# Performance work log

Measured on AMD Instinct MI355X. Metric: run time of the kernel, lower is better.

The kernel has to match this reference:

```python
import jax, jax.numpy as jnp
import numpy as np
from jax import lax

KS = 5            # patch kernel size
STRIDE = 4        # patch stride / scale ratio
SHIFTS = (2, 2)   # roll shifts before patch extraction
SOFTMAX_SCALE = 10.0
MID_CH = 64
BAND_HS = 8


def same_pad(x, k, s):
    """TensorFlow-style SAME padding for kernel k, stride s (NCHW)."""
    H, W = x.shape[-2], x.shape[-1]
    oh, ow = -(-H // s), -(-W // s)
    ph = max(0, (oh - 1) * s + k - H)
    pw = max(0, (ow - 1) * s + k - W)
    return jnp.pad(x, ((0, 0), (0, 0), (ph // 2, ph - ph // 2), (pw // 2, pw - pw // 2)))


def extract_patches(x, k, s, shifts):
    """torch.nn.Unfold equivalent with SAME padding and roll -> [N, L, C, k, k]."""
    x = same_pad(x, k, s)
    x = jnp.roll(x, shifts[0], axis=2)
    x = jnp.roll(x, shifts[1], axis=3)
    p = lax.conv_general_dilated_patches(
        x, (k, k), (s, s), 'VALID', dimension_numbers=('NCHW', 'OIHW', 'NCHW'))
    N, _, Hn, Wn = p.shape
    C = x.shape[1]
    # channel ordering is (C, kh, kw) channel-slowest, matching torch unfold
    return p.reshape(N, C, k, k, Hn * Wn).transpose(0, 4, 1, 2, 3)


def conv3(x, w, b):
    """3x3 conv, padding=1, bias + LeakyReLU(0.01) (BasicBlock)."""
    y = lax.conv_general_dilated(x, w, (1, 1), [(1, 1), (1, 1)],
                                 dimension_numbers=('NCHW', 'OIHW', 'NCHW'))
    return jax.nn.leaky_relu(y + b[None, :, None, None], 0.01)


def setup_inputs() -> dict:
    key = jax.random.key(0)
    ks = jax.random.split(key, 11)
    f32 = jnp.float32
    return {
        'ms':   jax.random.normal(ks[0], (2, BAND_HS, 96, 96), f32),
        'pan':  jax.random.normal(ks[1], (2, 1, 384, 384), f32),
        'pan2': jax.random.normal(ks[2], (2, 1, 96, 96), f32),
        'wq': jax.random.normal(ks[3], (MID_CH, 1, 3, 3), f32) * 0.1,
        'bq': jax.random.normal(ks[4], (MID_CH,), f32) * 0.02,
        'wk': jax.random.normal(ks[5], (MID_CH, 1, 3, 3), f32) * 0.1,
        'bk': jax.random.normal(ks[6], (MID_CH,), f32) * 0.02,
        'wv': jax.random.normal(ks[7], (BAND_HS, BAND_HS, 3, 3), f32) * 0.1,
        'bv': jax.random.normal(ks[8], (BAND_HS,), f32) * 0.02,
        'wr': jax.random.normal(ks[9], (BAND_HS, BAND_HS, 3, 3), f32) * 0.1,
        'br': jax.random.normal(ks[10], (BAND_HS,), f32) * 0.02,
    }


def reference(ms, pan, pan2, wq, bq, wk, bk, wv, bv, wr, br):
    k_fea = conv3(pan2, wk, bk)                       # [N, mid, h, w]
    q_fea = conv3(pan, wq, bq)                        # [N, mid, H, W]
    v_fea = conv3(ms, wv, bv)                         # [N, band, h, w]

    k_patch = extract_patches(k_fea, KS, STRIDE, SHIFTS)  # [N, L, mid, ks, ks]
    v_patch = extract_patches(v_fea, KS, STRIDE, SHIFTS)  # [N, L, band, ks, ks]

    def attend(q, kp, vp):
        # q: [mid, H, W]; kp: [L, mid, ks, ks]; vp: [L, band, ks, ks]
        norms = jnp.sqrt(jnp.sum(kp * kp, axis=(1, 2, 3)))      # per-patch L2 norms
        k0 = kp / jnp.max(norms)                                # global-max normalization
        q0 = same_pad(q[None], KS, STRIDE)                      # [1, mid, Hp, Wp]
        scores = lax.conv_general_dilated(
            q0, k0, (STRIDE, STRIDE), 'VALID',
            dimension_numbers=('NCHW', 'OIHW', 'NCHW'))          # [1, L, H', W']
        attn = jax.nn.softmax(scores * SOFTMAX_SCALE, axis=1)
        # conv_transpose2d(attn, vp, stride) == dilated conv with flipped, transposed kernel
        wT = jnp.flip(vp, (2, 3)).transpose(1, 0, 2, 3)          # [band, L, ks, ks]
        out = lax.conv_general_dilated(
            attn, wT, (1, 1), [(KS - 1, KS - 1)] * 2,
            lhs_dilation=(STRIDE, STRIDE),
            dimension_numbers=('NCHW', 'OIHW', 'NCHW'))          # [1, band, Ho, Wo]
        return out[0] / 6.0

    res = jax.vmap(attend)(q_fea, k_patch, v_patch)   # [N, band, Ho, Wo]
    return conv3(res, wr, br)
```

## Files before the change

### kernel.cpp

```cpp
#include <hip/hip_runtime.h>
#include <math.h>


typedef _Float16 f16;
typedef _Float16 f16x8 __attribute__((ext_vector_type(8)));
typedef float f32x4 __attribute__((ext_vector_type(4)));

namespace csa {
constexpr int NB   = 2;
constexpr int MID  = 64;
constexpr int BAND = 8;
constexpr int HK   = 96;
constexpr int HQ   = 384;
constexpr int HQP  = 385;
constexpr int XI   = 97;
constexpr int LN   = 24;
constexpr int L    = 576;
constexpr int LP   = 640;
constexpr int PS   = 96 * 96;
constexpr int KDIM = MID * 25;
constexpr int VDIM = BAND * 25;
constexpr int MV   = 256;
constexpr int HO   = 385;
constexpr size_t QPSN = (size_t)4 * HQP * XI * MID;

constexpr size_t align256(size_t x) { return (x + 255) & ~(size_t)255; }
constexpr size_t OFF_QPS  = 0;
constexpr size_t OFF_KCL  = align256(OFF_QPS + (size_t)NB*QPSN*2);
constexpr size_t OFF_VFEA = align256(OFF_KCL + (size_t)NB*HK*HK*MID*2);
constexpr size_t OFF_N2   = align256(OFF_VFEA + (size_t)NB*BAND*HK*HK*4);
constexpr size_t OFF_SC   = align256(OFF_N2   + (size_t)NB*L*4);
constexpr size_t OFF_KM   = align256(OFF_SC   + 256);
constexpr size_t OFF_VT   = align256(OFF_KM   + (size_t)NB*LP*KDIM*2);
constexpr size_t OFF_ST   = align256(OFF_VT   + (size_t)NB*MV*L*2);
constexpr size_t OFF_AT   = align256(OFF_ST   + (size_t)NB*PS*LP*4);
constexpr size_t OFF_D    = align256(OFF_AT   + (size_t)NB*PS*L*2);
constexpr size_t OFF_RES  = align256(OFF_D    + (size_t)NB*MV*PS*4);
}
using namespace csa;

__global__ __launch_bounds__(256) void csa_convq_ps(
    const float* __restrict__ in, const float* __restrict__ w,
    const float* __restrict__ b, f16* __restrict__ out) {
  int id = blockIdx.x * 256 + threadIdx.x;
  int total = NB * 4 * HQP * XI;
  if (id >= total) return;
  int xi = id % XI;
  int t = id / XI;
  int yp = t % HQP;
  t /= HQP;
  int f = t % 4;
  int n = t / 4;
  int xp = 4 * xi + f;
  f16* op = out + (size_t)id * MID;
  if (yp >= HQ || xp >= HQ) {
    f16x8 z = {0, 0, 0, 0, 0, 0, 0, 0};
#pragma unroll
    for (int c8 = 0; c8 < 8; ++c8) *(f16x8*)(op + c8 * 8) = z;
    return;
  }
  const float* ip = in + (size_t)n * HQ * HQ;
  float p[9];
#pragma unroll
  for (int dy = 0; dy < 3; ++dy)
#pragma unroll
    for (int dx = 0; dx < 3; ++dx) {
      int yy = yp + dy - 1, xx = xp + dx - 1;
      p[dy * 3 + dx] = (yy >= 0 && yy < HQ && xx >= 0 && xx < HQ)
                           ? ip[(size_t)yy * HQ + xx] : 0.f;
    }
#pragma unroll
  for (int c8 = 0; c8 < 8; ++c8) {
    f16x8 o;
#pragma unroll
    for (int e = 0; e < 8; ++e) {
      int co = c8 * 8 + e;
      float acc = b[co];
#pragma unroll
      for (int k = 0; k < 9; ++k) acc = fmaf(p[k], w[co * 9 + k], acc);
      o[e] = (f16)(acc > 0.f ? acc : 0.01f * acc);
    }
    *(f16x8*)(op + c8 * 8) = o;
  }
}

__global__ __launch_bounds__(256) void csa_conv_cl(
    const float* __restrict__ in, const float* __restrict__ w,
    const float* __restrict__ b, f16* __restrict__ out, int H) {
  int id = blockIdx.x * 256 + threadIdx.x;
  int total = NB * H * H;
  if (id >= total) return;
  int x = id % H;
  int t = id / H;
  int y = t % H;
  int n = t / H;
  f16* op = out + (size_t)id * MID;
  const float* ip = in + (size_t)n * H * H;
  float p[9];
#pragma unroll
  for (int dy = 0; dy < 3; ++dy)
#pragma unroll
    for (int dx = 0; dx < 3; ++dx) {
      int yy = y + dy - 1, xx = x + dx - 1;
      p[dy * 3 + dx] = (yy >= 0 && yy < H && xx >= 0 && xx < H)
                           ? ip[(size_t)yy * H + xx] : 0.f;
    }
#pragma unroll
  for (int c8 = 0; c8 < 8; ++c8) {
    f16x8 o;
#pragma unroll
    for (int e = 0; e < 8; ++e) {
      int co = c8 * 8 + e;
      float acc = b[co];
#pragma unroll
      for (int k = 0; k < 9; ++k) acc = fmaf(p[k], w[co * 9 + k], acc);
      o[e] = (f16)(acc > 0.f ? acc : 0.01f * acc);
    }
    *(f16x8*)(op + c8 * 8) = o;
  }
}

__global__ __launch_bounds__(256) void csa_conv3_8x8(
    const float* __restrict__ in, const float* __restrict__ w,
    const float* __restrict__ b, float* __restrict__ out, int H, int W) {
  int id = blockIdx.x * 256 + threadIdx.x;
  int total = NB * H * W;
  if (id >= total) return;
  int x = id % W;
  int t = id / W;
  int y = t % H;
  int n = t / H;
  const float* ip = in + (size_t)n * BAND * H * W;
  float p[BAND][9];
#pragma unroll
  for (int ci = 0; ci < BAND; ++ci)
#pragma unroll
    for (int dy = 0; dy < 3; ++dy)
#pragma unroll
      for (int dx = 0; dx < 3; ++dx) {
        int yy = y + dy - 1, xx = x + dx - 1;
        p[ci][dy * 3 + dx] = (yy >= 0 && yy < H && xx >= 0 && xx < W)
                                 ? ip[((size_t)ci * H + yy) * W + xx] : 0.f;
      }
  float* op = out + ((size_t)n * BAND * H + y) * W + x;
  for (int co = 0; co < BAND; ++co) {
    float acc = b[co];
#pragma unroll
    for (int ci = 0; ci < BAND; ++ci)
#pragma unroll
      for (int k = 0; k < 9; ++k)
        acc = fmaf(p[ci][k], w[(co * BAND + ci) * 9 + k], acc);
    acc = acc > 0.f ? acc : 0.01f * acc;
    op[(size_t)co * H * W] = acc;
  }
}

__global__ __launch_bounds__(256) void csa_build_patches(
    const f16* __restrict__ kcl, const float* __restrict__ v_fea,
    f16* __restrict__ Kmat, f16* __restrict__ Vt, float* __restrict__ n2) {
  int blk = blockIdx.x;
  int n = blk / LP;
  int l = blk % LP;
  int tid = threadIdx.x;
  f16* krow = Kmat + ((size_t)n * LP + l) * KDIM;
  if (l >= L) {
    f16x8 z = {0, 0, 0, 0, 0, 0, 0, 0};
    for (int ch = tid; ch < 200; ch += 256) *(f16x8*)(krow + ch * 8) = z;
    return;
  }
  int i = l / LN, j = l % LN;
  const f16* kn = kcl + (size_t)n * HK * HK * MID;
  float ss = 0.f;
  for (int ch = tid; ch < 200; ch += 256) {
    int khkw = ch >> 3;
    int c0 = (ch & 7) * 8;
    int kh = khkw / 5, kw = khkw % 5;
    int r = (4 * i + kh + 95) % 97;
    int cc = (4 * j + kw + 95) % 97;
    f16x8 v = {0, 0, 0, 0, 0, 0, 0, 0};
    if (r < HK && cc < HK)
      v = *(const f16x8*)(kn + ((size_t)r * HK + cc) * MID + c0);
#pragma unroll
    for (int e = 0; e < 8; ++e) {
      float fv = (float)v[e];
      ss += fv * fv;
    }
    *(f16x8*)(krow + ch * 8) = v;
  }
  for (int m = tid; m < MV; m += 256) {
    float v = 0.f;
    if (m < VDIM) {
      int kw = m % 5;
      int t = m / 5;
      int kh = t % 5;
      int c = t / 5;
      int r = (4 * i + kh + 95) % 97;
      int cc = (4 * j + kw + 95) % 97;
      v = (r < HK && cc < HK)
              ? v_fea[(((size_t)n * BAND + c) * HK + r) * HK + cc] : 0.f;
    }
    Vt[((size_t)n * MV + m) * L + l] = (f16)v;
  }
  __shared__ float red[256];
  red[tid] = ss;
  __syncthreads();
  for (int s = 128; s > 0; s >>= 1) {
    if (tid < s) red[tid] += red[tid + s];
    __syncthreads();
  }
  if (tid == 0) n2[n * L + l] = red[0];
}

__global__ __launch_bounds__(256) void csa_max_scale(
    const float* __restrict__ n2, float* __restrict__ scale) {
  int n = blockIdx.x;
  int tid = threadIdx.x;
  float m = 0.f;
  for (int l = tid; l < L; l += 256) m = fmaxf(m, n2[n * L + l]);
  __shared__ float red[256];
  red[tid] = m;
  __syncthreads();
  for (int s = 128; s > 0; s >>= 1) {
    if (tid < s) red[tid] = fmaxf(red[tid], red[tid + s]);
    __syncthreads();
  }
  if (tid == 0) scale[n] = 10.f / sqrtf(red[0]);
}

__device__ __forceinline__ void gl_lds16(const f16* g, f16* s) {
  __builtin_amdgcn_global_load_lds(
      (const __attribute__((address_space(1))) void*)g,
      (__attribute__((address_space(3))) void*)s, 16, 0, 0);
}

__global__ __launch_bounds__(256) void csa_gemm1(
    const f16* __restrict__ qps, const f16* __restrict__ Km,
    float* __restrict__ C) {
  __shared__ __attribute__((aligned(16))) f16 As[4096];
  __shared__ __attribute__((aligned(16))) f16 Bs[4096];
  const int tid = threadIdx.x;
  const int w = tid >> 6;
  const int l = tid & 63;
  const int q = l >> 4;
  const int r = l & 15;
  const int nb = blockIdx.z;
  qps += (size_t)nb * QPSN;
  Km += (size_t)nb * LP * KDIM;
  C += (size_t)nb * (size_t)PS * LP;
  const int bm = blockIdx.y * 128;
  const int bn = blockIdx.x * 128;
  const int wm = (w >> 1) * 64;
  const int wn = (w & 1) * 64;

  f32x4 acc[4][4];
#pragma unroll
  for (int i = 0; i < 4; ++i)
#pragma unroll
    for (int j = 0; j < 4; ++j) {
      f32x4 z = {0.f, 0.f, 0.f, 0.f};
      acc[i][j] = z;
    }

  const int pg0 = bm + w * 16;
  const int y0 = pg0 / 96, x0 = pg0 % 96;
  const int pg1 = pg0 + 64;
  const int y1 = pg1 / 96, x1 = pg1 % 96;
  const int la = r * MID + q * 8;

  const f16* gb0 = Km + (size_t)(bn + w * 16 + r) * KDIM + q * 8;
  const f16* gb1 = gb0 + (size_t)64 * KDIM;
  f16* lA0 = As + w * 512;
  f16* lA1 = As + 2048 + w * 512;
  f16* lB0 = Bs + w * 512;
  f16* lB1 = Bs + 2048 + w * 512;
  const int am = (w >> 1) * 4;
  const int bnn = (w & 1) * 4;

  int t = 0;
  for (int kh = 0; kh < 5; ++kh) {
    for (int kw = 0; kw < 5; ++kw) {
      const size_t u0 =
          (((size_t)(kw & 3) * HQP + (4 * y0 + kh)) * XI + x0 + (kw >> 2)) * MID;
      const size_t u1 =
          (((size_t)(kw & 3) * HQP + (4 * y1 + kh)) * XI + x1 + (kw >> 2)) * MID;
#pragma unroll
      for (int half = 0; half < 2; ++half, ++t) {
        const size_t oA = (size_t)half * 32 + la;
        const size_t oB = (size_t)t * 32;
        gl_lds16(qps + u0 + oA, lA0);
        gl_lds16(qps + u1 + oA, lA1);
        gl_lds16(gb0 + oB, lB0);
        gl_lds16(gb1 + oB, lB1);
        __syncthreads();
        f16x8 af[4], bf[4];
#pragma unroll
        for (int u = 0; u < 4; ++u) {
          af[u] = *(const f16x8*)&As[(am + u) * 512 + q * 128 + r * 8];
          bf[u] = *(const f16x8*)&Bs[(bnn + u) * 512 + q * 128 + r * 8];
        }
#pragma unroll
        for (int i = 0; i < 4; ++i)
#pragma unroll
          for (int j = 0; j < 4; ++j)
            acc[i][j] = __builtin_amdgcn_mfma_f32_16x16x32_f16(af[i], bf[j],
                                                               acc[i][j], 0, 0, 0);
        __syncthreads();
      }
    }
  }
  const int cn = bn + wn + r;
#pragma unroll
  for (int i = 0; i < 4; ++i) {
    int rm = bm + wm + i * 16 + q * 4;
#pragma unroll
    for (int j = 0; j < 4; ++j)
#pragma unroll
      for (int rr = 0; rr < 4; ++rr)
        C[(size_t)(rm + rr) * LP + cn + j * 16] = acc[i][j][rr];
  }
}

__global__ __launch_bounds__(256) void csa_gemm_f16(
    const f16* __restrict__ A, const f16* __restrict__ Bt,
    float* __restrict__ C, int M, int N, int K,
    size_t strideA, size_t strideB, size_t strideC) {
  __shared__ __attribute__((aligned(16))) f16 As[4096];
  __shared__ __attribute__((aligned(16))) f16 Bs[4096];
  const int tid = threadIdx.x;
  const int w = tid >> 6;
  const int l = tid & 63;
  const int q = l >> 4;
  const int r = l & 15;
  const int nb = blockIdx.z;
  A += (size_t)nb * strideA;
  Bt += (size_t)nb * strideB;
  C += (size_t)nb * strideC;
  const int bm = blockIdx.y * 128;
  const int bn = blockIdx.x * 128;
  const int wm = (w >> 1) * 64;
  const int wn = (w & 1) * 64;

  f32x4 acc[4][4];
#pragma unroll
  for (int i = 0; i < 4; ++i)
#pragma unroll
    for (int j = 0; j < 4; ++j) {
      f32x4 z = {0.f, 0.f, 0.f, 0.f};
      acc[i][j] = z;
    }

  const f16* ga0 = A + (size_t)(bm + w * 16 + r) * K + q * 8;
  const f16* ga1 = ga0 + (size_t)64 * K;
  const f16* gb0 = Bt + (size_t)(bn + w * 16 + r) * K + q * 8;
  const f16* gb1 = gb0 + (size_t)64 * K;
  f16* lA0 = As + w * 512;
  f16* lA1 = As + 2048 + w * 512;
  f16* lB0 = Bs + w * 512;
  f16* lB1 = Bs + 2048 + w * 512;
  const int am = (w >> 1) * 4;
  const int bnn = (w & 1) * 4;

  for (int k0 = 0; k0 < K; k0 += 32) {
    gl_lds16(ga0 + k0, lA0);
    gl_lds16(ga1 + k0, lA1);
    gl_lds16(gb0 + k0, lB0);
    gl_lds16(gb1 + k0, lB1);
    __syncthreads();
    f16x8 af[4], bf[4];
#pragma unroll
    for (int u = 0; u < 4; ++u) {
      af[u] = *(const f16x8*)&As[(am + u) * 512 + q * 128 + r * 8];
      bf[u] = *(const f16x8*)&Bs[(bnn + u) * 512 + q * 128 + r * 8];
    }
#pragma unroll
    for (int i = 0; i < 4; ++i)
#pragma unroll
      for (int j = 0; j < 4; ++j)
        acc[i][j] =
            __builtin_amdgcn_mfma_f32_16x16x32_f16(af[i], bf[j], acc[i][j], 0, 0, 0);
    __syncthreads();
  }

  const int cn = bn + wn + r;
#pragma unroll
  for (int i = 0; i < 4; ++i) {
    int rm = bm + wm + i * 16 + q * 4;
#pragma unroll
    for (int j = 0; j < 4; ++j)
#pragma unroll
      for (int rr = 0; rr < 4; ++rr)
        C[(size_t)(rm + rr) * N + cn + j * 16] = acc[i][j][rr];
  }
}

__global__ __launch_bounds__(256) void csa_softmax(
    const float* __restrict__ scoresT, const float* __restrict__ scale,
    f16* __restrict__ attnT) {
  const int wv = threadIdx.x >> 6;
  const int lane = threadIdx.x & 63;
  const int p = blockIdx.x * 4 + wv;
  const int n = blockIdx.y;
  const float sc = scale[n];
  const float* row = scoresT + ((size_t)n * PS + p) * LP;
  float v[9];
  float m = -1e30f;
#pragma unroll
  for (int j = 0; j < 9; ++j) {
    v[j] = row[lane + j * 64] * sc;
    m = fmaxf(m, v[j]);
  }
#pragma unroll
  for (int off = 32; off > 0; off >>= 1) m = fmaxf(m, __shfl_xor(m, off));
  float e[9], s = 0.f;
#pragma unroll
  for (int j = 0; j < 9; ++j) {
    e[j] = __expf(v[j] - m);
    s += e[j];
  }
#pragma unroll
  for (int off = 32; off > 0; off >>= 1) s += __shfl_xor(s, off);
  const float inv = 1.f / s;
  f16* orow = attnT + ((size_t)n * PS + p) * L;
#pragma unroll
  for (int j = 0; j < 9; ++j) orow[lane + j * 64] = (f16)(e[j] * inv);
}

__global__ __launch_bounds__(256) void csa_gather(
    const float* __restrict__ D, float* __restrict__ res) {
  int id = blockIdx.x * 256 + threadIdx.x;
  if (id >= NB * BAND * HO * HO) return;
  int ox = id % HO;
  int t = id / HO;
  int oy = t % HO;
  t = t / HO;
  int co = t % BAND;
  int n = t / BAND;
  const float* Dn = D + (size_t)n * MV * PS;
  float s = 0.f;
  int kh0 = oy & 3;
  int kw0 = ox & 3;
  for (int kh = kh0; kh < 5; kh += 4) {
    int y = (oy - kh) >> 2;
    if (y < 0 || y >= 96) continue;
    for (int kw = kw0; kw < 5; kw += 4) {
      int x = (ox - kw) >> 2;
      if (x < 0 || x >= 96) continue;
      s += Dn[(size_t)(co * 25 + kh * 5 + kw) * PS + y * 96 + x];
    }
  }
  res[id] = s * (1.f / 6.f);
}

extern "C" void kernel_launch(void* const* d_in, const int* in_sizes, int n_in,
                              void* d_out, int out_size, void* d_ws,
                              size_t ws_size, hipStream_t stream) {
  const float* ms   = (const float*)d_in[0];
  const float* pan  = (const float*)d_in[1];
  const float* pan2 = (const float*)d_in[2];
  const float* wq = (const float*)d_in[3];
  const float* bq = (const float*)d_in[4];
  const float* wk = (const float*)d_in[5];
  const float* bk = (const float*)d_in[6];
  const float* wv = (const float*)d_in[7];
  const float* bv = (const float*)d_in[8];
  const float* wr = (const float*)d_in[9];
  const float* br = (const float*)d_in[10];
  float* out = (float*)d_out;

  char* ws = (char*)d_ws;
  f16*   qps   = (f16*)(ws + OFF_QPS);
  f16*   kcl   = (f16*)(ws + OFF_KCL);
  float* v_fea = (float*)(ws + OFF_VFEA);
  float* n2    = (float*)(ws + OFF_N2);
  float* scale = (float*)(ws + OFF_SC);
  f16*   Kmat  = (f16*)(ws + OFF_KM);
  f16*   Vt    = (f16*)(ws + OFF_VT);
  float* scoT  = (float*)(ws + OFF_ST);
  f16*   attnT = (f16*)(ws + OFF_AT);
  float* Dm    = (float*)(ws + OFF_D);
  float* res   = (float*)(ws + OFF_RES);

  dim3 b256(256);
  csa_convq_ps<<<dim3((NB * 4 * HQP * XI + 255) / 256), b256, 0, stream>>>(
      pan, wq, bq, qps);
  csa_conv_cl<<<dim3((NB * HK * HK + 255) / 256), b256, 0, stream>>>(
      pan2, wk, bk, kcl, HK);
  csa_conv3_8x8<<<dim3((NB * HK * HK + 255) / 256), b256, 0, stream>>>(
      ms, wv, bv, v_fea, HK, HK);
  csa_build_patches<<<dim3(NB * LP), b256, 0, stream>>>(kcl, v_fea, Kmat, Vt,
                                                        n2);
  csa_max_scale<<<dim3(NB), b256, 0, stream>>>(n2, scale);

  csa_gemm1<<<dim3(LP / 128, PS / 128, NB), b256, 0, stream>>>(qps, Kmat,
                                                               scoT);

  csa_softmax<<<dim3(PS / 4, NB), b256, 0, stream>>>(scoT, scale, attnT);

  csa_gemm_f16<<<dim3(PS / 128, MV / 128, NB), b256, 0, stream>>>(
      Vt, attnT, Dm, MV, PS, L,
      (size_t)MV * L, (size_t)PS * L, (size_t)MV * PS);

  csa_gather<<<dim3((NB * BAND * HO * HO + 255) / 256), b256, 0, stream>>>(
      Dm, res);
  csa_conv3_8x8<<<dim3((NB * HO * HO + 255) / 256), b256, 0, stream>>>(
      res, wr, br, out, HO, HO);
}
```

Before: 279.4 us.

## Fuse score GEMM, softmax and value GEMM into one flash-style attention kernel

Replaces the separate score GEMM, softmax and value GEMM kernels with one kernel per 32-pixel tile. The kernel computes all 576 scores in registers, does the softmax with LDS reductions, stores unnormalized f16 probabilities in LDS and multiplies by Vt. This removes the large fp32 score matrix and the f16 attention matrix round trips through global memory. The D buffer is also switched to f16 and the padded L rows are dropped. The trade-off is that K and V fragments are read directly from global memory without LDS staging, with fewer blocks and lower data reuse per block.

Result: slower. 379.4 us (+35.8%).

```diff
diff --git a/kernel.cpp b/kernel.cpp
--- a/kernel.cpp
+++ b/kernel.cpp
@@ -16,12 +16,13 @@
 constexpr int XI   = 97;
 constexpr int LN   = 24;
 constexpr int L    = 576;
-constexpr int LP   = 640;
 constexpr int PS   = 96 * 96;
 constexpr int KDIM = MID * 25;
 constexpr int VDIM = BAND * 25;
 constexpr int MV   = 256;
 constexpr int HO   = 385;
+constexpr int TP   = 32;
+constexpr int PADL = 584;
 constexpr size_t QPSN = (size_t)4 * HQP * XI * MID;
 
 constexpr size_t align256(size_t x) { return (x + 255) & ~(size_t)255; }
@@ -31,11 +32,9 @@
 constexpr size_t OFF_N2   = align256(OFF_VFEA + (size_t)NB*BAND*HK*HK*4);
 constexpr size_t OFF_SC   = align256(OFF_N2   + (size_t)NB*L*4);
 constexpr size_t OFF_KM   = align256(OFF_SC   + 256);
-constexpr size_t OFF_VT   = align256(OFF_KM   + (size_t)NB*LP*KDIM*2);
-constexpr size_t OFF_ST   = align256(OFF_VT   + (size_t)NB*MV*L*2);
-constexpr size_t OFF_AT   = align256(OFF_ST   + (size_t)NB*PS*LP*4);
-constexpr size_t OFF_D    = align256(OFF_AT   + (size_t)NB*PS*L*2);
-constexpr size_t OFF_RES  = align256(OFF_D    + (size_t)NB*MV*PS*4);
+constexpr size_t OFF_VT   = align256(OFF_KM   + (size_t)NB*L*KDIM*2);
+constexpr size_t OFF_D    = align256(OFF_VT   + (size_t)NB*MV*L*2);
+constexpr size_t OFF_RES  = align256(OFF_D    + (size_t)NB*MV*PS*2);
 }
 using namespace csa;
 
@@ -159,15 +158,10 @@
     const f16* __restrict__ kcl, const float* __restrict__ v_fea,
     f16* __restrict__ Kmat, f16* __restrict__ Vt, float* __restrict__ n2) {
   int blk = blockIdx.x;
-  int n = blk / LP;
-  int l = blk % LP;
+  int n = blk / L;
+  int l = blk % L;
   int tid = threadIdx.x;
-  f16* krow = Kmat + ((size_t)n * LP + l) * KDIM;
-  if (l >= L) {
-    f16x8 z = {0, 0, 0, 0, 0, 0, 0, 0};
-    for (int ch = tid; ch < 200; ch += 256) *(f16x8*)(krow + ch * 8) = z;
-    return;
-  }
+  f16* krow = Kmat + ((size_t)n * L + l) * KDIM;
   int i = l / LN, j = l % LN;
   const f16* kn = kcl + (size_t)n * HK * HK * MID;
   float ss = 0.f;
@@ -233,200 +227,165 @@
       (__attribute__((address_space(3))) void*)s, 16, 0, 0);
 }
 
-__global__ __launch_bounds__(256) void csa_gemm1(
+__global__ __launch_bounds__(256) void csa_attn(
     const f16* __restrict__ qps, const f16* __restrict__ Km,
-    float* __restrict__ C) {
-  __shared__ __attribute__((aligned(16))) f16 As[4096];
-  __shared__ __attribute__((aligned(16))) f16 Bs[4096];
+    const f16* __restrict__ Vt, const float* __restrict__ scale,
+    f16* __restrict__ D) {
+  __shared__ __attribute__((aligned(16))) f16 shb[13 * 2048];
+  __shared__ float mtile[4][TP];
+  __shared__ float stile[4][TP];
+  __shared__ float mrow[TP];
+  __shared__ float linv[TP];
+
   const int tid = threadIdx.x;
   const int w = tid >> 6;
-  const int l = tid & 63;
-  const int q = l >> 4;
-  const int r = l & 15;
-  const int nb = blockIdx.z;
+  const int q = (tid >> 4) & 3;
+  const int r = tid & 15;
+  const int nb = blockIdx.y;
+  const int p0 = blockIdx.x * TP;
+  const float sc = scale[nb];
   qps += (size_t)nb * QPSN;
-  Km += (size_t)nb * LP * KDIM;
-  C += (size_t)nb * (size_t)PS * LP;
-  const int bm = blockIdx.y * 128;
-  const int bn = blockIdx.x * 128;
-  const int wm = (w >> 1) * 64;
-  const int wn = (w & 1) * 64;
-
-  f32x4 acc[4][4];
+  Km += (size_t)nb * (size_t)L * KDIM;
+  Vt += (size_t)nb * (size_t)MV * L;
+  D += (size_t)nb * (size_t)MV * PS;
+
+  const int y0 = p0 / 96, x0 = p0 % 96;
+  const int s_c = w >> 1, s_kk = w & 1;
+  const int qoff_t = (x0 + 16 * s_c + r) * MID + s_kk * 32 + q * 8;
+
+  f32x4 sacc[2][9];
+#pragma unroll
+  for (int c = 0; c < 2; ++c)
+#pragma unroll
+    for (int j = 0; j < 9; ++j) {
+      f32x4 z = {0.f, 0.f, 0.f, 0.f};
+      sacc[c][j] = z;
+    }
+
+  const f16* kb = Km + (size_t)(144 * w + r) * KDIM + q * 8;
+
+  for (int h = 0; h < 2; ++h) {
+    const int t0 = h ? 13 : 0;
+    const int nt = h ? 12 : 13;
+    if (h) __syncthreads();
+    for (int tl = 0; tl < nt; ++tl) {
+      const int t = t0 + tl;
+      const int kh = t / 5, kw = t % 5;
+      const size_t qb =
+          (((size_t)(kw & 3) * HQP + (4 * y0 + kh)) * XI + (kw >> 2)) * MID;
+      gl_lds16(qps + qb + qoff_t, shb + tl * 2048 + w * 512);
+    }
+    __syncthreads();
+#pragma unroll 1
+    for (int tl = 0; tl < nt; ++tl) {
+      const int t = t0 + tl;
+#pragma unroll
+      for (int kk = 0; kk < 2; ++kk) {
+        f16x8 af0 = *(const f16x8*)&shb[tl * 2048 + kk * 512 + q * 128 + r * 8];
+        f16x8 af1 =
+            *(const f16x8*)&shb[tl * 2048 + (2 + kk) * 512 + q * 128 + r * 8];
+        f16x8 bf[9];
+#pragma unroll
+        for (int j = 0; j < 9; ++j)
+          bf[j] = *(const f16x8*)(kb + (size_t)j * 16 * KDIM + t * 64 + kk * 32);
+#pragma unroll
+        for (int j = 0; j < 9; ++j) {
+          sacc[0][j] =
+              __builtin_amdgcn_mfma_f32_16x16x32_f16(af0, bf[j], sacc[0][j], 0, 0, 0);
+          sacc[1][j] =
+              __builtin_amdgcn_mfma_f32_16x16x32_f16(af1, bf[j], sacc[1][j], 0, 0, 0);
+        }
+      }
+    }
+  }
+
+#pragma unroll
+  for (int c = 0; c < 2; ++c)
+#pragma unroll
+    for (int rr = 0; rr < 4; ++rr) {
+      float mx = -1e30f;
+#pragma unroll
+      for (int j = 0; j < 9; ++j) {
+        float v = sacc[c][j][rr] * sc;
+        sacc[c][j][rr] = v;
+        mx = fmaxf(mx, v);
+      }
+      mx = fmaxf(mx, __shfl_xor(mx, 1));
+      mx = fmaxf(mx, __shfl_xor(mx, 2));
+      mx = fmaxf(mx, __shfl_xor(mx, 4));
+      mx = fmaxf(mx, __shfl_xor(mx, 8));
+      if (r == 0) mtile[w][16 * c + 4 * q + rr] = mx;
+    }
+  __syncthreads();
+  if (tid < TP)
+    mrow[tid] = fmaxf(fmaxf(mtile[0][tid], mtile[1][tid]),
+                      fmaxf(mtile[2][tid], mtile[3][tid]));
+  __syncthreads();
+
+#pragma unroll
+  for (int c = 0; c < 2; ++c)
+#pragma unroll
+    for (int rr = 0; rr < 4; ++rr) {
+      const int pl = 16 * c + 4 * q + rr;
+      const float m = mrow[pl];
+      float s = 0.f;
+#pragma unroll
+      for (int j = 0; j < 9; ++j) {
+        float e = __expf(sacc[c][j][rr] - m);
+        s += e;
+        shb[pl * PADL + 144 * w + 16 * j + r] = (f16)e;
+      }
+      s += __shfl_xor(s, 1);
+      s += __shfl_xor(s, 2);
+      s += __shfl_xor(s, 4);
+      s += __shfl_xor(s, 8);
+      if (r == 0) stile[w][pl] = s;
+    }
+  __syncthreads();
+  if (tid < TP)
+    linv[tid] =
+        1.f / (stile[0][tid] + stile[1][tid] + stile[2][tid] + stile[3][tid]);
+  __syncthreads();
+
+  f32x4 oacc[4][2];
 #pragma unroll
   for (int i = 0; i < 4; ++i)
 #pragma unroll
-    for (int j = 0; j < 4; ++j) {
+    for (int jp = 0; jp < 2; ++jp) {
       f32x4 z = {0.f, 0.f, 0.f, 0.f};
-      acc[i][j] = z;
-    }
-
-  const int pg0 = bm + w * 16;
-  const int y0 = pg0 / 96, x0 = pg0 % 96;
-  const int pg1 = pg0 + 64;
-  const int y1 = pg1 / 96, x1 = pg1 % 96;
-  const int la = r * MID + q * 8;
-
-  const f16* gb0 = Km + (size_t)(bn + w * 16 + r) * KDIM + q * 8;
-  const f16* gb1 = gb0 + (size_t)64 * KDIM;
-  f16* lA0 = As + w * 512;
-  f16* lA1 = As + 2048 + w * 512;
-  f16* lB0 = Bs + w * 512;
-  f16* lB1 = Bs + 2048 + w * 512;
-  const int am = (w >> 1) * 4;
-  const int bnn = (w & 1) * 4;
-
-  int t = 0;
-  for (int kh = 0; kh < 5; ++kh) {
-    for (int kw = 0; kw < 5; ++kw) {
-      const size_t u0 =
-          (((size_t)(kw & 3) * HQP + (4 * y0 + kh)) * XI + x0 + (kw >> 2)) * MID;
-      const size_t u1 =
-          (((size_t)(kw & 3) * HQP + (4 * y1 + kh)) * XI + x1 + (kw >> 2)) * MID;
-#pragma unroll
-      for (int half = 0; half < 2; ++half, ++t) {
-        const size_t oA = (size_t)half * 32 + la;
-        const size_t oB = (size_t)t * 32;
-        gl_lds16(qps + u0 + oA, lA0);
-        gl_lds16(qps + u1 + oA, lA1);
-        gl_lds16(gb0 + oB, lB0);
-        gl_lds16(gb1 + oB, lB1);
-        __syncthreads();
-        f16x8 af[4], bf[4];
-#pragma unroll
-        for (int u = 0; u < 4; ++u) {
-          af[u] = *(const f16x8*)&As[(am + u) * 512 + q * 128 + r * 8];
-          bf[u] = *(const f16x8*)&Bs[(bnn + u) * 512 + q * 128 + r * 8];
-        }
-#pragma unroll
-        for (int i = 0; i < 4; ++i)
-#pragma unroll
-          for (int j = 0; j < 4; ++j)
-            acc[i][j] = __builtin_amdgcn_mfma_f32_16x16x32_f16(af[i], bf[j],
-                                                               acc[i][j], 0, 0, 0);
-        __syncthreads();
+      oacc[i][jp] = z;
+    }
+  const f16* vb = Vt + (size_t)(64 * w + r) * L + q * 8;
+#pragma unroll 1
+  for (int rd = 0; rd < 9; ++rd) {
+#pragma unroll
+    for (int kk = 0; kk < 2; ++kk) {
+      const int lo = rd * 64 + kk * 32 + q * 8;
+      f16x8 pf0 = *(const f16x8*)&shb[r * PADL + lo];
+      f16x8 pf1 = *(const f16x8*)&shb[(16 + r) * PADL + lo];
+#pragma unroll
+      for (int i = 0; i < 4; ++i) {
+        f16x8 vf = *(const f16x8*)(vb + (size_t)i * 16 * L + rd * 64 + kk * 32);
+        oacc[i][0] =
+            __builtin_amdgcn_mfma_f32_16x16x32_f16(vf, pf0, oacc[i][0], 0, 0, 0);
+        oacc[i][1] =
+            __builtin_amdgcn_mfma_f32_16x16x32_f16(vf, pf1, oacc[i][1], 0, 0, 0);
       }
     }
   }
-  const int cn = bn + wn + r;
-#pragma unroll
-  for (int i = 0; i < 4; ++i) {
-    int rm = bm + wm + i * 16 + q * 4;
-#pragma unroll
-    for (int j = 0; j < 4; ++j)
-#pragma unroll
-      for (int rr = 0; rr < 4; ++rr)
-        C[(size_t)(rm + rr) * LP + cn + j * 16] = acc[i][j][rr];
-  }
-}
-
-__global__ __launch_bounds__(256) void csa_gemm_f16(
-    const f16* __restrict__ A, const f16* __restrict__ Bt,
-    float* __restrict__ C, int M, int N, int K,
-    size_t strideA, size_t strideB, size_t strideC) {
-  __shared__ __attribute__((aligned(16))) f16 As[4096];
-  __shared__ __attribute__((aligned(16))) f16 Bs[4096];
-  const int tid = threadIdx.x;
-  const int w = tid >> 6;
-  const int l = tid & 63;
-  const int q = l >> 4;
-  const int r = l & 15;
-  const int nb = blockIdx.z;
-  A += (size_t)nb * strideA;
-  Bt += (size_t)nb * strideB;
-  C += (size_t)nb * strideC;
-  const int bm = blockIdx.y * 128;
-  const int bn = blockIdx.x * 128;
-  const int wm = (w >> 1) * 64;
-  const int wn = (w & 1) * 64;
-
-  f32x4 acc[4][4];
+  const float li0 = linv[r], li1 = linv[16 + r];
 #pragma unroll
   for (int i = 0; i < 4; ++i)
 #pragma unroll
-    for (int j = 0; j < 4; ++j) {
-      f32x4 z = {0.f, 0.f, 0.f, 0.f};
-      acc[i][j] = z;
-    }
-
-  const f16* ga0 = A + (size_t)(bm + w * 16 + r) * K + q * 8;
-  const f16* ga1 = ga0 + (size_t)64 * K;
-  const f16* gb0 = Bt + (size_t)(bn + w * 16 + r) * K + q * 8;
-  const f16* gb1 = gb0 + (size_t)64 * K;
-  f16* lA0 = As + w * 512;
-  f16* lA1 = As + 2048 + w * 512;
-  f16* lB0 = Bs + w * 512;
-  f16* lB1 = Bs + 2048 + w * 512;
-  const int am = (w >> 1) * 4;
-  const int bnn = (w & 1) * 4;
-
-  for (int k0 = 0; k0 < K; k0 += 32) {
-    gl_lds16(ga0 + k0, lA0);
-    gl_lds16(ga1 + k0, lA1);
-    gl_lds16(gb0 + k0, lB0);
-    gl_lds16(gb1 + k0, lB1);
-    __syncthreads();
-    f16x8 af[4], bf[4];
-#pragma unroll
-    for (int u = 0; u < 4; ++u) {
-      af[u] = *(const f16x8*)&As[(am + u) * 512 + q * 128 + r * 8];
-      bf[u] = *(const f16x8*)&Bs[(bnn + u) * 512 + q * 128 + r * 8];
-    }
-#pragma unroll
-    for (int i = 0; i < 4; ++i)
-#pragma unroll
-      for (int j = 0; j < 4; ++j)
-        acc[i][j] =
-            __builtin_amdgcn_mfma_f32_16x16x32_f16(af[i], bf[j], acc[i][j], 0, 0, 0);
-    __syncthreads();
-  }
-
-  const int cn = bn + wn + r;
-#pragma unroll
-  for (int i = 0; i < 4; ++i) {
-    int rm = bm + wm + i * 16 + q * 4;
-#pragma unroll
-    for (int j = 0; j < 4; ++j)
-#pragma unroll
-      for (int rr = 0; rr < 4; ++rr)
-        C[(size_t)(rm + rr) * N + cn + j * 16] = acc[i][j][rr];
-  }
-}
-
-__global__ __launch_bounds__(256) void csa_softmax(
-    const float* __restrict__ scoresT, const float* __restrict__ scale,
-    f16* __restrict__ attnT) {
-  const int wv = threadIdx.x >> 6;
-  const int lane = threadIdx.x & 63;
-  const int p = blockIdx.x * 4 + wv;
-  const int n = blockIdx.y;
-  const float sc = scale[n];
-  const float* row = scoresT + ((size_t)n * PS + p) * LP;
-  float v[9];
-  float m = -1e30f;
-#pragma unroll
-  for (int j = 0; j < 9; ++j) {
-    v[j] = row[lane + j * 64] * sc;
-    m = fmaxf(m, v[j]);
-  }
-#pragma unroll
-  for (int off = 32; off > 0; off >>= 1) m = fmaxf(m, __shfl_xor(m, off));
-  float e[9], s = 0.f;
-#pragma unroll
-  for (int j = 0; j < 9; ++j) {
-    e[j] = __expf(v[j] - m);
-    s += e[j];
-  }
-#pragma unroll
-  for (int off = 32; off > 0; off >>= 1) s += __shfl_xor(s, off);
-  const float inv = 1.f / s;
-  f16* orow = attnT + ((size_t)n * PS + p) * L;
-#pragma unroll
-  for (int j = 0; j < 9; ++j) orow[lane + j * 64] = (f16)(e[j] * inv);
+    for (int rr = 0; rr < 4; ++rr) {
+      const int m = 64 * w + 16 * i + 4 * q + rr;
+      D[(size_t)m * PS + p0 + r] = (f16)(oacc[i][0][rr] * li0);
+      D[(size_t)m * PS + p0 + 16 + r] = (f16)(oacc[i][1][rr] * li1);
+    }
 }
 
 __global__ __launch_bounds__(256) void csa_gather(
-    const float* __restrict__ D, float* __restrict__ res) {
+    const f16* __restrict__ D, float* __restrict__ res) {
   int id = blockIdx.x * 256 + threadIdx.x;
   if (id >= NB * BAND * HO * HO) return;
   int ox = id % HO;
@@ -435,7 +394,7 @@
   t = t / HO;
   int co = t % BAND;
   int n = t / BAND;
-  const float* Dn = D + (size_t)n * MV * PS;
+  const f16* Dn = D + (size_t)n * MV * PS;
   float s = 0.f;
   int kh0 = oy & 3;
   int kw0 = ox & 3;
@@ -445,7 +404,7 @@
     for (int kw = kw0; kw < 5; kw += 4) {
       int x = (ox - kw) >> 2;
       if (x < 0 || x >= 96) continue;
-      s += Dn[(size_t)(co * 25 + kh * 5 + kw) * PS + y * 96 + x];
+      s += (float)Dn[(size_t)(co * 25 + kh * 5 + kw) * PS + y * 96 + x];
     }
   }
   res[id] = s * (1.f / 6.f);
@@ -475,9 +434,7 @@
   float* scale = (float*)(ws + OFF_SC);
   f16*   Kmat  = (f16*)(ws + OFF_KM);
   f16*   Vt    = (f16*)(ws + OFF_VT);
-  float* scoT  = (float*)(ws + OFF_ST);
-  f16*   attnT = (f16*)(ws + OFF_AT);
-  float* Dm    = (float*)(ws + OFF_D);
+  f16*   Dm    = (f16*)(ws + OFF_D);
   float* res   = (float*)(ws + OFF_RES);
 
   dim3 b256(256);
@@ -487,18 +444,11 @@
       pan2, wk, bk, kcl, HK);
   csa_conv3_8x8<<<dim3((NB * HK * HK + 255) / 256), b256, 0, stream>>>(
       ms, wv, bv, v_fea, HK, HK);
-  csa_build_patches<<<dim3(NB * LP), b256, 0, stream>>>(kcl, v_fea, Kmat, Vt,
-                                                        n2);
+  csa_build_patches<<<dim3(NB * L), b256, 0, stream>>>(kcl, v_fea, Kmat, Vt,
+                                                       n2);
   csa_max_scale<<<dim3(NB), b256, 0, stream>>>(n2, scale);
 
-  csa_gemm1<<<dim3(LP / 128, PS / 128, NB), b256, 0, stream>>>(qps, Kmat,
-                                                               scoT);
-
-  csa_softmax<<<dim3(PS / 4, NB), b256, 0, stream>>>(scoT, scale, attnT);
-
-  csa_gemm_f16<<<dim3(PS / 128, MV / 128, NB), b256, 0, stream>>>(
-      Vt, attnT, Dm, MV, PS, L,
-      (size_t)MV * L, (size_t)PS * L, (size_t)MV * PS);
+  csa_attn<<<dim3(PS / TP, NB), b256, 0, stream>>>(qps, Kmat, Vt, scale, Dm);
 
   csa_gather<<<dim3((NB * BAND * HO * HO + 255) / 256), b256, 0, stream>>>(
       Dm, res);
```

## Retile score GEMM to 64x128, deepen K-steps to 64, store D in fp16

Applied to the files above, without the earlier changes.

The score GEMM now uses 64-row M tiles, which doubles the block count to 720, and loads a full 64-channel K slice per (kh,kw) tap. That halves the barriers per tap. The second GEMM also moves to K=64 per iteration with twice the LDS, and writes its output D in fp16 instead of fp32, halving the traffic into the gather kernel. In exchange, the first GEMM reuses each B tile less, and the fp16 intermediate costs some precision.

Result: slower. 308.3 us (+10.4%).

```diff
diff --git a/kernel.cpp b/kernel.cpp
--- a/kernel.cpp
+++ b/kernel.cpp
@@ -35,7 +35,7 @@
 constexpr size_t OFF_ST   = align256(OFF_VT   + (size_t)NB*MV*L*2);
 constexpr size_t OFF_AT   = align256(OFF_ST   + (size_t)NB*PS*LP*4);
 constexpr size_t OFF_D    = align256(OFF_AT   + (size_t)NB*PS*L*2);
-constexpr size_t OFF_RES  = align256(OFF_D    + (size_t)NB*MV*PS*4);
+constexpr size_t OFF_RES  = align256(OFF_D    + (size_t)NB*MV*PS*2);
 }
 using namespace csa;
 
@@ -237,7 +237,7 @@
     const f16* __restrict__ qps, const f16* __restrict__ Km,
     float* __restrict__ C) {
   __shared__ __attribute__((aligned(16))) f16 As[4096];
-  __shared__ __attribute__((aligned(16))) f16 Bs[4096];
+  __shared__ __attribute__((aligned(16))) f16 Bs[8192];
   const int tid = threadIdx.x;
   const int w = tid >> 6;
   const int l = tid & 63;
@@ -245,72 +245,69 @@
   const int r = l & 15;
   const int nb = blockIdx.z;
   qps += (size_t)nb * QPSN;
-  Km += (size_t)nb * LP * KDIM;
+  Km += (size_t)nb * (size_t)LP * KDIM;
   C += (size_t)nb * (size_t)PS * LP;
-  const int bm = blockIdx.y * 128;
+  const int bm = blockIdx.y * 64;
   const int bn = blockIdx.x * 128;
-  const int wm = (w >> 1) * 64;
+  const int wm = (w >> 1) * 32;
   const int wn = (w & 1) * 64;
 
-  f32x4 acc[4][4];
-#pragma unroll
-  for (int i = 0; i < 4; ++i)
+  f32x4 acc[2][4];
+#pragma unroll
+  for (int i = 0; i < 2; ++i)
 #pragma unroll
     for (int j = 0; j < 4; ++j) {
       f32x4 z = {0.f, 0.f, 0.f, 0.f};
       acc[i][j] = z;
     }
 
-  const int pg0 = bm + w * 16;
-  const int y0 = pg0 / 96, x0 = pg0 % 96;
-  const int pg1 = pg0 + 64;
-  const int y1 = pg1 / 96, x1 = pg1 % 96;
+  const int pg = bm + w * 16;
+  const int y0 = pg / 96, x0 = pg % 96;
   const int la = r * MID + q * 8;
 
   const f16* gb0 = Km + (size_t)(bn + w * 16 + r) * KDIM + q * 8;
   const f16* gb1 = gb0 + (size_t)64 * KDIM;
-  f16* lA0 = As + w * 512;
-  f16* lA1 = As + 2048 + w * 512;
-  f16* lB0 = Bs + w * 512;
-  f16* lB1 = Bs + 2048 + w * 512;
-  const int am = (w >> 1) * 4;
+  f16* lA = As + w * 1024;
+  f16* lB0 = Bs + w * 1024;
+  f16* lB1 = Bs + 4096 + w * 1024;
+  const int am = (w >> 1) * 2;
   const int bnn = (w & 1) * 4;
 
-  int t = 0;
   for (int kh = 0; kh < 5; ++kh) {
+#pragma unroll
     for (int kw = 0; kw < 5; ++kw) {
-      const size_t u0 =
-          (((size_t)(kw & 3) * HQP + (4 * y0 + kh)) * XI + x0 + (kw >> 2)) * MID;
-      const size_t u1 =
-          (((size_t)(kw & 3) * HQP + (4 * y1 + kh)) * XI + x1 + (kw >> 2)) * MID;
-#pragma unroll
-      for (int half = 0; half < 2; ++half, ++t) {
-        const size_t oA = (size_t)half * 32 + la;
-        const size_t oB = (size_t)t * 32;
-        gl_lds16(qps + u0 + oA, lA0);
-        gl_lds16(qps + u1 + oA, lA1);
-        gl_lds16(gb0 + oB, lB0);
-        gl_lds16(gb1 + oB, lB1);
-        __syncthreads();
-        f16x8 af[4], bf[4];
-#pragma unroll
-        for (int u = 0; u < 4; ++u) {
-          af[u] = *(const f16x8*)&As[(am + u) * 512 + q * 128 + r * 8];
-          bf[u] = *(const f16x8*)&Bs[(bnn + u) * 512 + q * 128 + r * 8];
-        }
-#pragma unroll
-        for (int i = 0; i < 4; ++i)
+      const size_t u =
+          (((size_t)(kw & 3) * HQP + (4 * y0 + kh)) * XI + x0 + (kw >> 2)) * MID + la;
+      const size_t oB = (size_t)(kh * 5 + kw) * 64;
+      gl_lds16(qps + u, lA);
+      gl_lds16(qps + u + 32, lA + 512);
+      gl_lds16(gb0 + oB, lB0);
+      gl_lds16(gb0 + oB + 32, lB0 + 512);
+      gl_lds16(gb1 + oB, lB1);
+      gl_lds16(gb1 + oB + 32, lB1 + 512);
+      __syncthreads();
+#pragma unroll
+      for (int kk = 0; kk < 2; ++kk) {
+        f16x8 af[2], bf[4];
+#pragma unroll
+        for (int i = 0; i < 2; ++i)
+          af[i] = *(const f16x8*)&As[(am + i) * 1024 + kk * 512 + q * 128 + r * 8];
+#pragma unroll
+        for (int j = 0; j < 4; ++j)
+          bf[j] = *(const f16x8*)&Bs[(bnn + j) * 1024 + kk * 512 + q * 128 + r * 8];
+#pragma unroll
+        for (int i = 0; i < 2; ++i)
 #pragma unroll
           for (int j = 0; j < 4; ++j)
             acc[i][j] = __builtin_amdgcn_mfma_f32_16x16x32_f16(af[i], bf[j],
                                                                acc[i][j], 0, 0, 0);
-        __syncthreads();
       }
+      __syncthreads();
     }
   }
   const int cn = bn + wn + r;
 #pragma unroll
-  for (int i = 0; i < 4; ++i) {
+  for (int i = 0; i < 2; ++i) {
     int rm = bm + wm + i * 16 + q * 4;
 #pragma unroll
     for (int j = 0; j < 4; ++j)
@@ -320,12 +317,12 @@
   }
 }
 
-__global__ __launch_bounds__(256) void csa_gemm_f16(
+__global__ __launch_bounds__(256) void csa_gemm2(
     const f16* __restrict__ A, const f16* __restrict__ Bt,
-    float* __restrict__ C, int M, int N, int K,
+    f16* __restrict__ C, int M, int N, int K,
     size_t strideA, size_t strideB, size_t strideC) {
-  __shared__ __attribute__((aligned(16))) f16 As[4096];
-  __shared__ __attribute__((aligned(16))) f16 Bs[4096];
+  __shared__ __attribute__((aligned(16))) f16 As[8192];
+  __shared__ __attribute__((aligned(16))) f16 Bs[8192];
   const int tid = threadIdx.x;
   const int w = tid >> 6;
   const int l = tid & 63;
@@ -353,31 +350,38 @@
   const f16* ga1 = ga0 + (size_t)64 * K;
   const f16* gb0 = Bt + (size_t)(bn + w * 16 + r) * K + q * 8;
   const f16* gb1 = gb0 + (size_t)64 * K;
-  f16* lA0 = As + w * 512;
-  f16* lA1 = As + 2048 + w * 512;
-  f16* lB0 = Bs + w * 512;
-  f16* lB1 = Bs + 2048 + w * 512;
+  f16* lA0 = As + w * 1024;
+  f16* lA1 = As + 4096 + w * 1024;
+  f16* lB0 = Bs + w * 1024;
+  f16* lB1 = Bs + 4096 + w * 1024;
   const int am = (w >> 1) * 4;
   const int bnn = (w & 1) * 4;
 
-  for (int k0 = 0; k0 < K; k0 += 32) {
+  for (int k0 = 0; k0 < K; k0 += 64) {
     gl_lds16(ga0 + k0, lA0);
+    gl_lds16(ga0 + k0 + 32, lA0 + 512);
     gl_lds16(ga1 + k0, lA1);
+    gl_lds16(ga1 + k0 + 32, lA1 + 512);
     gl_lds16(gb0 + k0, lB0);
+    gl_lds16(gb0 + k0 + 32, lB0 + 512);
     gl_lds16(gb1 + k0, lB1);
+    gl_lds16(gb1 + k0 + 32, lB1 + 512);
     __syncthreads();
-    f16x8 af[4], bf[4];
-#pragma unroll
-    for (int u = 0; u < 4; ++u) {
-      af[u] = *(const f16x8*)&As[(am + u) * 512 + q * 128 + r * 8];
-      bf[u] = *(const f16x8*)&Bs[(bnn + u) * 512 + q * 128 + r * 8];
-    }
-#pragma unroll
-    for (int i = 0; i < 4; ++i)
-#pragma unroll
-      for (int j = 0; j < 4; ++j)
-        acc[i][j] =
-            __builtin_amdgcn_mfma_f32_16x16x32_f16(af[i], bf[j], acc[i][j], 0, 0, 0);
+#pragma unroll
+    for (int kk = 0; kk < 2; ++kk) {
+      f16x8 af[4], bf[4];
+#pragma unroll
+      for (int u = 0; u < 4; ++u) {
+        af[u] = *(const f16x8*)&As[(am + u) * 1024 + kk * 512 + q * 128 + r * 8];
+        bf[u] = *(const f16x8*)&Bs[(bnn + u) * 1024 + kk * 512 + q * 128 + r * 8];
+      }
+#pragma unroll
+      for (int i = 0; i < 4; ++i)
+#pragma unroll
+        for (int j = 0; j < 4; ++j)
+          acc[i][j] = __builtin_amdgcn_mfma_f32_16x16x32_f16(af[i], bf[j],
+                                                             acc[i][j], 0, 0, 0);
+    }
     __syncthreads();
   }
 
@@ -389,7 +393,7 @@
     for (int j = 0; j < 4; ++j)
 #pragma unroll
       for (int rr = 0; rr < 4; ++rr)
-        C[(size_t)(rm + rr) * N + cn + j * 16] = acc[i][j][rr];
+        C[(size_t)(rm + rr) * N + cn + j * 16] = (f16)acc[i][j][rr];
   }
 }
 
@@ -426,7 +430,7 @@
 }
 
 __global__ __launch_bounds__(256) void csa_gather(
-    const float* __restrict__ D, float* __restrict__ res) {
+    const f16* __restrict__ D, float* __restrict__ res) {
   int id = blockIdx.x * 256 + threadIdx.x;
   if (id >= NB * BAND * HO * HO) return;
   int ox = id % HO;
@@ -435,7 +439,7 @@
   t = t / HO;
   int co = t % BAND;
   int n = t / BAND;
-  const float* Dn = D + (size_t)n * MV * PS;
+  const f16* Dn = D + (size_t)n * MV * PS;
   float s = 0.f;
   int kh0 = oy & 3;
   int kw0 = ox & 3;
@@ -445,7 +449,7 @@
     for (int kw = kw0; kw < 5; kw += 4) {
       int x = (ox - kw) >> 2;
       if (x < 0 || x >= 96) continue;
-      s += Dn[(size_t)(co * 25 + kh * 5 + kw) * PS + y * 96 + x];
+      s += (float)Dn[(size_t)(co * 25 + kh * 5 + kw) * PS + y * 96 + x];
     }
   }
   res[id] = s * (1.f / 6.f);
@@ -477,7 +481,7 @@
   f16*   Vt    = (f16*)(ws + OFF_VT);
   float* scoT  = (float*)(ws + OFF_ST);
   f16*   attnT = (f16*)(ws + OFF_AT);
-  float* Dm    = (float*)(ws + OFF_D);
+  f16*   Dm    = (f16*)(ws + OFF_D);
   float* res   = (float*)(ws + OFF_RES);
 
   dim3 b256(256);
@@ -491,12 +495,11 @@
                                                         n2);
   csa_max_scale<<<dim3(NB), b256, 0, stream>>>(n2, scale);
 
-  csa_gemm1<<<dim3(LP / 128, PS / 128, NB), b256, 0, stream>>>(qps, Kmat,
-                                                               scoT);
+  csa_gemm1<<<dim3(LP / 128, PS / 64, NB), b256, 0, stream>>>(qps, Kmat, scoT);
 
   csa_softmax<<<dim3(PS / 4, NB), b256, 0, stream>>>(scoT, scale, attnT);
 
-  csa_gemm_f16<<<dim3(PS / 128, MV / 128, NB), b256, 0, stream>>>(
+  csa_gemm2<<<dim3(PS / 128, MV / 128, NB), b256, 0, stream>>>(
       Vt, attnT, Dm, MV, PS, L,
       (size_t)MV * L, (size_t)PS * L, (size_t)MV * PS);
 
```
